# Kernel optimization log

Hardware: AMD Instinct MI355X
Metric: run time of the kernel (lower is better)

## Reference

```python
import jax, jax.numpy as jnp
import numpy as np

NUM_HEADS = 32
HEAD_DIM = 32  # hard-coded in the module


def _rope_sincos(seq_len, head_dim):
    # NOTE: module uses arange(0, head_dim)/head_dim (full dim, not the usual /2 stride)
    inv_freq = 1.0 / (10000.0 ** (jnp.arange(0, head_dim, dtype=jnp.float32) / head_dim))
    freqs = jnp.outer(jnp.arange(seq_len, dtype=jnp.float32), inv_freq)  # [S, D]
    # original repeats over heads then reshapes -> identical values per head,
    # so broadcasting with shape [1, S, 1, D] is equivalent.
    return jnp.sin(freqs)[None, :, None, :], jnp.cos(freqs)[None, :, None, :]


def _apply_rope(x, sin, cos):
    x1, x2 = jnp.split(x, 2, axis=-1)
    x_rot = jnp.concatenate([-x2, x1], axis=-1)
    return x * cos + x_rot * sin


def setup_inputs() -> dict:
    key = jax.random.key(0)
    B, S, H, D = 2, 2048, NUM_HEADS, HEAD_DIM
    dm = H * D
    k1, k2 = jax.random.split(key)
    x = jax.random.normal(k1, (B, S, dm), dtype=jnp.float32)
    W_qkv = jax.random.normal(k2, (dm, 3 * dm), dtype=jnp.float32) / np.sqrt(dm).astype(np.float32)
    mask = jnp.tril(jnp.ones((S, S), dtype=bool))[None, None]  # causal, [1,1,S,S]
    return {"x": x, "W_qkv": W_qkv, "mask": mask}


def reference(x, W_qkv, mask):
    B, S, dm = x.shape
    H, D = NUM_HEADS, HEAD_DIM
    qkv = x @ W_qkv  # [B, S, 3*H*D], no bias
    q, k, v = jnp.split(qkv, 3, axis=-1)
    q = q.reshape(B, S, H, D)
    k = k.reshape(B, S, H, D)
    v = v.reshape(B, S, H, D)

    sin, cos = _rope_sincos(S, D)
    q = _apply_rope(q, sin, cos)
    k = _apply_rope(k, sin, cos)

    # [B, H, S, D]
    q = q.transpose(0, 2, 1, 3)
    k = k.transpose(0, 2, 1, 3)
    v = v.transpose(0, 2, 1, 3)

    scale = 1.0 / np.sqrt(D).astype(np.float32)
    attn = jnp.einsum('bhqd,bhkd->bhqk', q, k) * scale  # [B, H, S, S]
    attn = jnp.where(mask, attn, jnp.float32(-jnp.inf))
    attn = jax.nn.softmax(attn, axis=-1)
    out = jnp.einsum('bhqk,bhkd->bhqd', attn, v)  # [B, H, S, D]
    return out.transpose(0, 2, 1, 3).reshape(B, S, H * D)
```

## Files before the change

kernel.cpp:

```cpp
#include <hip/hip_runtime.h>
#include <cstdint>
#include <cstddef>

#define BB 2
#define SS 2048
#define HH 32
#define DD 32
#define DM 1024
#define MROWS 4096
#define NQKV 3072

#define QSCALE 0.25503486f

typedef __attribute__((ext_vector_type(8))) short bf16x8;
typedef __attribute__((ext_vector_type(4))) float f32x4;
typedef __attribute__((address_space(1))) unsigned int gu32;
typedef __attribute__((address_space(3))) unsigned int lu32;

__device__ __forceinline__ unsigned short f2bf(float f) {
    union { float f; unsigned int u; } v;
    v.f = f;
    unsigned int u = v.u;
    u += 0x7fffu + ((u >> 16) & 1u);
    return (unsigned short)(u >> 16);
}

__device__ __forceinline__ unsigned int cvt_pk_bf16(float a, float b) {
    unsigned int r;
    asm("v_cvt_pk_bf16_f32 %0, %1, %2" : "=v"(r) : "v"(a), "v"(b));
    return r;
}
__device__ __forceinline__ unsigned short bf1(float a) {
    return (unsigned short)cvt_pk_bf16(a, a);
}

__global__ __launch_bounds__(256) void prep_k(
        const float* __restrict__ x, const float* __restrict__ w,
        unsigned short* __restrict__ xb, unsigned short* __restrict__ wT,
        float* __restrict__ tk, float* __restrict__ tq) {
    __shared__ unsigned short tile[64][65];
    const int blk = blockIdx.x;
    const int tid = threadIdx.x;
    if (blk < 4096) {
        const int i = blk * 256 + tid;
        float4 v = ((const float4*)x)[i];
        ushort4 o;
        o.x = f2bf(v.x); o.y = f2bf(v.y); o.z = f2bf(v.z); o.w = f2bf(v.w);
        ((ushort4*)xb)[i] = o;
    } else if (blk < 4864) {
        const int bx = blk - 4096;
        const int n0 = (bx % 48) * 64;
        const int k0 = (bx / 48) * 64;
        const int tx = tid & 63;
        const int ty = tid >> 6;
        for (int i = ty; i < 64; i += 4)
            tile[i][tx] = f2bf(w[(size_t)(k0 + i) * NQKV + n0 + tx]);
        __syncthreads();
        for (int i = ty; i < 64; i += 4)
            wT[(size_t)(n0 + i) * 1024 + k0 + tx] = tile[tx][i];
    } else {
        const int i = (blk - 4864) * 256 + tid;
        const int s = i >> 4, dl = i & 15;
        const float inv1 = exp2f((float)dl * -0.41524101186092029f);
        const float inv2 = exp2f((float)(dl + 16) * -0.41524101186092029f);
        float s1, c1, s2, c2;
        sincosf((float)s * inv1, &s1, &c1);
        sincosf((float)s * inv2, &s2, &c2);
        float4 vk = {s1, c1, s2, c2};
        float4 vq = {s1 * QSCALE, c1 * QSCALE, s2 * QSCALE, c2 * QSCALE};
        ((float4*)tk)[i] = vk;
        ((float4*)tq)[i] = vq;
    }
}

__global__ __launch_bounds__(256) void qkv_gemm_k(
        const unsigned short* __restrict__ xb,
        const unsigned short* __restrict__ wTp,
        const float4* __restrict__ tk, const float4* __restrict__ tq,
        unsigned short* __restrict__ qbuf,
        unsigned short* __restrict__ kbuf,
        unsigned short* __restrict__ vtbuf) {
    __shared__ unsigned short smem[2 * 8192];
    const int m0 = blockIdx.x * 128;
    const int n0 = blockIdx.y * 128;
    const int tid = threadIdx.x;
    const int w = tid >> 6, lane = tid & 63;
    const int quad = lane >> 4, l16 = lane & 15;
    const int wr = w >> 1, wc = w & 1;

    f32x4 acc[4][4];
#pragma unroll
    for (int i = 0; i < 4; ++i)
#pragma unroll
        for (int j = 0; j < 4; ++j)
            acc[i][j] = (f32x4){0.f, 0.f, 0.f, 0.f};

    const int G = (lane & 56) | ((lane ^ (lane >> 3)) & 7);
    const int goff = (G >> 2) * 1024 + (G & 3) * 8;
    const int Gr = l16 * 4 + quad;
    const int L = Gr ^ ((Gr >> 3) & 7);
    const int roff = L * 8;

#define QKV_STAGE(k0, buf)                                                          \
    do {                                                                            \
        unsigned short* As_ = smem + (buf) * 8192;                                  \
        unsigned short* Bs_ = As_ + 4096;                                           \
        _Pragma("unroll")                                                           \
        for (int q = 0; q < 2; ++q) {                                               \
            const int seg = w * 2 + q;                                              \
            const unsigned short* ga = xb  + (size_t)(m0 + seg * 16) * 1024 + (k0) + goff; \
            const unsigned short* gb = wTp + (size_t)(n0 + seg * 16) * 1024 + (k0) + goff; \
            __builtin_amdgcn_global_load_lds((gu32*)ga, (lu32*)(As_ + seg * 512), 16, 0, 0); \
            __builtin_amdgcn_global_load_lds((gu32*)gb, (lu32*)(Bs_ + seg * 512), 16, 0, 0); \
        }                                                                           \
    } while (0)

    QKV_STAGE(0, 0);
    __syncthreads();
    int cur = 0;
    for (int kt = 0; kt < 32; ++kt) {
        if (kt < 31) QKV_STAGE((kt + 1) * 32, cur ^ 1);
        const unsigned short* As = smem + cur * 8192;
        const unsigned short* Bs = As + 4096;
        bf16x8 af[4], bfv[4];
#pragma unroll
        for (int i = 0; i < 4; ++i)
            af[i] = *(const bf16x8*)(As + (wr * 4 + i) * 512 + roff);
#pragma unroll
        for (int j = 0; j < 4; ++j)
            bfv[j] = *(const bf16x8*)(Bs + (wc * 4 + j) * 512 + roff);
#pragma unroll
        for (int i = 0; i < 4; ++i)
#pragma unroll
            for (int j = 0; j < 4; ++j)
                acc[i][j] = __builtin_amdgcn_mfma_f32_16x16x32_bf16(af[i], bfv[j], acc[i][j], 0, 0, 0);
        __syncthreads();
        cur ^= 1;
    }
#undef QKV_STAGE

    const int sec = n0 >> 10;
    const int rowb = m0 + wr * 64;
    const int colb = n0 + wc * 64;
    if (sec < 2) {
        unsigned short* dst = (sec == 0) ? qbuf : kbuf;
        const float4* tab = (sec == 0) ? tq : tk;
        const int h0 = (colb & 1023) >> 5;
        const int h1 = ((colb + 32) & 1023) >> 5;
#pragma unroll
        for (int i = 0; i < 4; ++i) {
#pragma unroll
            for (int r = 0; r < 4; ++r) {
                const int row = rowb + i * 16 + quad * 4 + r;
                const int bb = row >> 11, s = row & 2047;
                const float4 t = tab[s * 16 + l16];
                unsigned short* pb = dst + ((size_t)(bb * 32) * 2048 + s) * 32;
                {
                    const float x1 = acc[i][0][r], x2 = acc[i][1][r];
                    unsigned short* p = pb + (size_t)h0 * (2048 * 32);
                    p[l16]      = bf1(x1 * t.y - x2 * t.x);
                    p[l16 + 16] = bf1(x2 * t.w + x1 * t.z);
                }
                {
                    const float x1 = acc[i][2][r], x2 = acc[i][3][r];
                    unsigned short* p = pb + (size_t)h1 * (2048 * 32);
                    p[l16]      = bf1(x1 * t.y - x2 * t.x);
                    p[l16 + 16] = bf1(x2 * t.w + x1 * t.z);
                }
            }
        }
    } else {
        __syncthreads();
        unsigned short* tw = smem + w * 2048;
        const int bbi = rowb >> 11;
        const int srow = rowb & 2047;
        const int colB = colb - 2048;
#pragma unroll
        for (int j = 0; j < 4; ++j) {
#pragma unroll
            for (int i = 0; i < 4; ++i) {
                uint2 pk;
                pk.x = cvt_pk_bf16(acc[i][j][0], acc[i][j][1]);
                pk.y = cvt_pk_bf16(acc[i][j][2], acc[i][j][3]);
                *(uint2*)&tw[l16 * 66 + i * 16 + quad * 4] = pk;
            }
#pragma unroll
            for (int c = 0; c < 16; ++c) {
                const int col = colB + j * 16 + c;
                const int hh = col >> 5, d = col & 31;
                vtbuf[((size_t)(bbi * 32 + hh) * 32 + d) * 2048 + srow + lane] = tw[c * 66 + lane];
            }
        }
    }
}

__global__ __launch_bounds__(256) void attn_k(
        const unsigned short* __restrict__ qb,
        const unsigned short* __restrict__ kb,
        const unsigned short* __restrict__ vt,
        float* __restrict__ out) {
    __shared__ unsigned short Pl[4][2][32][40];
    const int tid = threadIdx.x;
    const int w = tid >> 6, lane = tid & 63;
    const int quad = lane >> 4, l16 = lane & 15;
    const int i = blockIdx.x;
    const int xcd = i & 7;
    const int slot = i >> 3;
    const int bh = ((slot & 7) << 3) | xcd;
    const int pr = slot >> 3;
    const int b = bh >> 5, h = bh & 31;

    const unsigned short* qbase = qb + (size_t)bh * 2048 * 32;
    const unsigned short* kbase = kb + (size_t)bh * 2048 * 32;
    const unsigned short* vbase = vt + (size_t)bh * 32 * 2048;
    const f32x4 fz = {0.f, 0.f, 0.f, 0.f};

    for (int ph = 0; ph < 2; ++ph) {
        const int qw = (ph == 0) ? (pr * 128 + w * 32)
                                 : ((15 - pr) * 128 + (3 - w) * 32);
        const int nkt = (qw >> 5) + 1;

        bf16x8 qf0 = *(const bf16x8*)(qbase + (size_t)(qw + l16) * 32 + quad * 8);
        bf16x8 qf1 = *(const bf16x8*)(qbase + (size_t)(qw + 16 + l16) * 32 + quad * 8);

        f32x4 a00 = fz, a01 = fz, a10 = fz, a11 = fz;
        float ls0 = 0.f, ls1 = 0.f;

        const unsigned short* kp0 = kbase + (size_t)l16 * 32 + quad * 8;
        const unsigned short* kp1 = kbase + (size_t)(16 + l16) * 32 + quad * 8;
        const unsigned short* vp0 = vbase + (size_t)l16 * 2048 + quad * 8;
        const unsigned short* vp1 = vbase + (size_t)(16 + l16) * 2048 + quad * 8;

        bf16x8 kc0 = *(const bf16x8*)kp0;
        bf16x8 kc1 = *(const bf16x8*)kp1;
        bf16x8 vc0 = *(const bf16x8*)vp0;
        bf16x8 vc1 = *(const bf16x8*)vp1;

        f32x4 s00 = __builtin_amdgcn_mfma_f32_16x16x32_bf16(kc0, qf0, fz, 0, 0, 0);
        f32x4 s01 = __builtin_amdgcn_mfma_f32_16x16x32_bf16(kc0, qf1, fz, 0, 0, 0);
        f32x4 s10 = __builtin_amdgcn_mfma_f32_16x16x32_bf16(kc1, qf0, fz, 0, 0, 0);
        f32x4 s11 = __builtin_amdgcn_mfma_f32_16x16x32_bf16(kc1, qf1, fz, 0, 0, 0);

        for (int kt = 0; kt < nkt - 1; ++kt) {
            kp0 += 1024; kp1 += 1024; vp0 += 32; vp1 += 32;
            bf16x8 kn0 = *(const bf16x8*)kp0;
            bf16x8 kn1 = *(const bf16x8*)kp1;
            bf16x8 vn0 = *(const bf16x8*)vp0;
            bf16x8 vn1 = *(const bf16x8*)vp1;

            unsigned short (*plw)[40] = Pl[w][kt & 1];
            {
                float p0 = __builtin_amdgcn_exp2f(s00[0]), p1 = __builtin_amdgcn_exp2f(s00[1]);
                float p2 = __builtin_amdgcn_exp2f(s00[2]), p3 = __builtin_amdgcn_exp2f(s00[3]);
                ls0 += (p0 + p1) + (p2 + p3);
                uint2 pk; pk.x = cvt_pk_bf16(p0, p1); pk.y = cvt_pk_bf16(p2, p3);
                *(uint2*)&plw[l16][quad * 4] = pk;
            }
            {
                float p0 = __builtin_amdgcn_exp2f(s01[0]), p1 = __builtin_amdgcn_exp2f(s01[1]);
                float p2 = __builtin_amdgcn_exp2f(s01[2]), p3 = __builtin_amdgcn_exp2f(s01[3]);
                ls1 += (p0 + p1) + (p2 + p3);
                uint2 pk; pk.x = cvt_pk_bf16(p0, p1); pk.y = cvt_pk_bf16(p2, p3);
                *(uint2*)&plw[16 + l16][quad * 4] = pk;
            }
            {
                float p0 = __builtin_amdgcn_exp2f(s10[0]), p1 = __builtin_amdgcn_exp2f(s10[1]);
                float p2 = __builtin_amdgcn_exp2f(s10[2]), p3 = __builtin_amdgcn_exp2f(s10[3]);
                ls0 += (p0 + p1) + (p2 + p3);
                uint2 pk; pk.x = cvt_pk_bf16(p0, p1); pk.y = cvt_pk_bf16(p2, p3);
                *(uint2*)&plw[l16][16 + quad * 4] = pk;
            }
            {
                float p0 = __builtin_amdgcn_exp2f(s11[0]), p1 = __builtin_amdgcn_exp2f(s11[1]);
                float p2 = __builtin_amdgcn_exp2f(s11[2]), p3 = __builtin_amdgcn_exp2f(s11[3]);
                ls1 += (p0 + p1) + (p2 + p3);
                uint2 pk; pk.x = cvt_pk_bf16(p0, p1); pk.y = cvt_pk_bf16(p2, p3);
                *(uint2*)&plw[16 + l16][16 + quad * 4] = pk;
            }

            bf16x8 pf0 = *(const bf16x8*)&plw[l16][quad * 8];
            bf16x8 pf1 = *(const bf16x8*)&plw[16 + l16][quad * 8];
            a00 = __builtin_amdgcn_mfma_f32_16x16x32_bf16(vc0, pf0, a00, 0, 0, 0);
            a01 = __builtin_amdgcn_mfma_f32_16x16x32_bf16(vc0, pf1, a01, 0, 0, 0);
            a10 = __builtin_amdgcn_mfma_f32_16x16x32_bf16(vc1, pf0, a10, 0, 0, 0);
            a11 = __builtin_amdgcn_mfma_f32_16x16x32_bf16(vc1, pf1, a11, 0, 0, 0);

            s00 = __builtin_amdgcn_mfma_f32_16x16x32_bf16(kn0, qf0, fz, 0, 0, 0);
            s01 = __builtin_amdgcn_mfma_f32_16x16x32_bf16(kn0, qf1, fz, 0, 0, 0);
            s10 = __builtin_amdgcn_mfma_f32_16x16x32_bf16(kn1, qf0, fz, 0, 0, 0);
            s11 = __builtin_amdgcn_mfma_f32_16x16x32_bf16(kn1, qf1, fz, 0, 0, 0);

            vc0 = vn0; vc1 = vn1;
        }

        {
            unsigned short (*plw)[40] = Pl[w][(nkt - 1) & 1];
            {
                float p[4];
#pragma unroll
                for (int r = 0; r < 4; ++r)
                    p[r] = (quad * 4 + r > l16) ? 0.f : __builtin_amdgcn_exp2f(s00[r]);
                ls0 += (p[0] + p[1]) + (p[2] + p[3]);
                uint2 pk; pk.x = cvt_pk_bf16(p[0], p[1]); pk.y = cvt_pk_bf16(p[2], p[3]);
                *(uint2*)&plw[l16][quad * 4] = pk;
            }
            {
                float p0 = __builtin_amdgcn_exp2f(s01[0]), p1 = __builtin_amdgcn_exp2f(s01[1]);
                float p2 = __builtin_amdgcn_exp2f(s01[2]), p3 = __builtin_amdgcn_exp2f(s01[3]);
                ls1 += (p0 + p1) + (p2 + p3);
                uint2 pk; pk.x = cvt_pk_bf16(p0, p1); pk.y = cvt_pk_bf16(p2, p3);
                *(uint2*)&plw[16 + l16][quad * 4] = pk;
            }
            {
                uint2 pk; pk.x = 0; pk.y = 0;
                *(uint2*)&plw[l16][16 + quad * 4] = pk;
            }
            {
                float p[4];
#pragma unroll
                for (int r = 0; r < 4; ++r)
                    p[r] = (quad * 4 + r > l16) ? 0.f : __builtin_amdgcn_exp2f(s11[r]);
                ls1 += (p[0] + p[1]) + (p[2] + p[3]);
                uint2 pk; pk.x = cvt_pk_bf16(p[0], p[1]); pk.y = cvt_pk_bf16(p[2], p[3]);
                *(uint2*)&plw[16 + l16][16 + quad * 4] = pk;
            }

            bf16x8 pf0 = *(const bf16x8*)&plw[l16][quad * 8];
            bf16x8 pf1 = *(const bf16x8*)&plw[16 + l16][quad * 8];
            a00 = __builtin_amdgcn_mfma_f32_16x16x32_bf16(vc0, pf0, a00, 0, 0, 0);
            a01 = __builtin_amdgcn_mfma_f32_16x16x32_bf16(vc0, pf1, a01, 0, 0, 0);
            a10 = __builtin_amdgcn_mfma_f32_16x16x32_bf16(vc1, pf0, a10, 0, 0, 0);
            a11 = __builtin_amdgcn_mfma_f32_16x16x32_bf16(vc1, pf1, a11, 0, 0, 0);
        }

        float l0 = ls0; l0 += __shfl_xor(l0, 16); l0 += __shfl_xor(l0, 32);
        float l1 = ls1; l1 += __shfl_xor(l1, 16); l1 += __shfl_xor(l1, 32);
        const float inv0 = 1.f / l0, inv1 = 1.f / l1;

        float* ot = (float*)&Pl[w][0][0][0];
        {
            f32x4 t;
            t = a00; t[0]*=inv0; t[1]*=inv0; t[2]*=inv0; t[3]*=inv0;
            *(f32x4*)&ot[(l16) * 36 + quad * 4] = t;
            t = a10; t[0]*=inv0; t[1]*=inv0; t[2]*=inv0; t[3]*=inv0;
            *(f32x4*)&ot[(l16) * 36 + 16 + quad * 4] = t;
            t = a01; t[0]*=inv1; t[1]*=inv1; t[2]*=inv1; t[3]*=inv1;
            *(f32x4*)&ot[(16 + l16) * 36 + quad * 4] = t;
            t = a11; t[0]*=inv1; t[1]*=inv1; t[2]*=inv1; t[3]*=inv1;
            *(f32x4*)&ot[(16 + l16) * 36 + 16 + quad * 4] = t;
        }
        const int dd = lane & 31, qpar = lane >> 5;
        float* ob = out + (size_t)(b * 2048 + qw) * 1024 + h * 32;
#pragma unroll
        for (int i2 = 0; i2 < 16; ++i2) {
            const int qloc = i2 * 2 + qpar;
            ob[(size_t)qloc * 1024 + dd] = ot[qloc * 36 + dd];
        }
    }
}

extern "C" void kernel_launch(void* const* d_in, const int* in_sizes, int n_in,
                              void* d_out, int out_size, void* d_ws, size_t ws_size,
                              hipStream_t stream) {
    (void)in_sizes; (void)n_in; (void)out_size; (void)ws_size;
    const float* x = (const float*)d_in[0];
    const float* wq = (const float*)d_in[1];
    float* out = (float*)d_out;

    unsigned short* xb = (unsigned short*)d_ws;
    unsigned short* wT = xb + (size_t)MROWS * DM;
    unsigned short* qb = wT + (size_t)NQKV * DM;
    unsigned short* kb = qb + (size_t)BB * HH * SS * DD;
    unsigned short* vt = kb + (size_t)BB * HH * SS * DD;
    float* tk = (float*)(vt + (size_t)BB * HH * SS * DD);
    float* tq = tk + (size_t)SS * 16 * 4;

    prep_k<<<dim3(4992), dim3(256), 0, stream>>>(x, wq, xb, wT, tk, tq);
    qkv_gemm_k<<<dim3(MROWS / 128, NQKV / 128), dim3(256), 0, stream>>>(
        xb, wT, (const float4*)tk, (const float4*)tq, qb, kb, vt);
    attn_k<<<dim3(BB * HH * 8), dim3(256), 0, stream>>>(qb, kb, vt, out);
}
```

Before: 178.9 us.

## Split attention key loop into two interleaved accumulator streams per wave

The attention inner loop now splits key tiles into two independent streams (even and odd tiles), each with its own accumulators, row sums, prefetch pointers and LDS P buffers. The two streams are interleaved so the MFMA, exp and LDS work of one can overlap with the other, and the partial results are summed at the end. The diagonal masked tile is handled by whichever stream owns it. This doubles accumulator and prefetch register pressure and LDS footprint, which may reduce occupancy.

```diff
diff --git a/kernel.cpp b/kernel.cpp
--- a/kernel.cpp
+++ b/kernel.cpp
@@ -194,12 +194,104 @@
     }
 }
 
+#define ATTN_TILE(KC0, KC1, VC0, VC1, KP0, KP1, VP0, VP1, A00, A01, A10, A11, LS0, LS1, PLW) \
+    {                                                                                \
+        KP0 += 2048; KP1 += 2048; VP0 += 64; VP1 += 64;                              \
+        bf16x8 kn0 = *(const bf16x8*)KP0;                                            \
+        bf16x8 kn1 = *(const bf16x8*)KP1;                                            \
+        bf16x8 vn0 = *(const bf16x8*)VP0;                                            \
+        bf16x8 vn1 = *(const bf16x8*)VP1;                                            \
+        f32x4 s00 = __builtin_amdgcn_mfma_f32_16x16x32_bf16(KC0, qf0, fz, 0, 0, 0);  \
+        f32x4 s01 = __builtin_amdgcn_mfma_f32_16x16x32_bf16(KC0, qf1, fz, 0, 0, 0);  \
+        f32x4 s10 = __builtin_amdgcn_mfma_f32_16x16x32_bf16(KC1, qf0, fz, 0, 0, 0);  \
+        f32x4 s11 = __builtin_amdgcn_mfma_f32_16x16x32_bf16(KC1, qf1, fz, 0, 0, 0);  \
+        unsigned short (*plw)[40] = PLW;                                             \
+        {                                                                            \
+            float p0 = __builtin_amdgcn_exp2f(s00[0]), p1 = __builtin_amdgcn_exp2f(s00[1]); \
+            float p2 = __builtin_amdgcn_exp2f(s00[2]), p3 = __builtin_amdgcn_exp2f(s00[3]); \
+            LS0 += (p0 + p1) + (p2 + p3);                                            \
+            uint2 pk; pk.x = cvt_pk_bf16(p0, p1); pk.y = cvt_pk_bf16(p2, p3);        \
+            *(uint2*)&plw[l16][quad * 4] = pk;                                       \
+        }                                                                            \
+        {                                                                            \
+            float p0 = __builtin_amdgcn_exp2f(s01[0]), p1 = __builtin_amdgcn_exp2f(s01[1]); \
+            float p2 = __builtin_amdgcn_exp2f(s01[2]), p3 = __builtin_amdgcn_exp2f(s01[3]); \
+            LS1 += (p0 + p1) + (p2 + p3);                                            \
+            uint2 pk; pk.x = cvt_pk_bf16(p0, p1); pk.y = cvt_pk_bf16(p2, p3);        \
+            *(uint2*)&plw[16 + l16][quad * 4] = pk;                                  \
+        }                                                                            \
+        {                                                                            \
+            float p0 = __builtin_amdgcn_exp2f(s10[0]), p1 = __builtin_amdgcn_exp2f(s10[1]); \
+            float p2 = __builtin_amdgcn_exp2f(s10[2]), p3 = __builtin_amdgcn_exp2f(s10[3]); \
+            LS0 += (p0 + p1) + (p2 + p3);                                            \
+            uint2 pk; pk.x = cvt_pk_bf16(p0, p1); pk.y = cvt_pk_bf16(p2, p3);        \
+            *(uint2*)&plw[l16][16 + quad * 4] = pk;                                  \
+        }                                                                            \
+        {                                                                            \
+            float p0 = __builtin_amdgcn_exp2f(s11[0]), p1 = __builtin_amdgcn_exp2f(s11[1]); \
+            float p2 = __builtin_amdgcn_exp2f(s11[2]), p3 = __builtin_amdgcn_exp2f(s11[3]); \
+            LS1 += (p0 + p1) + (p2 + p3);                                            \
+            uint2 pk; pk.x = cvt_pk_bf16(p0, p1); pk.y = cvt_pk_bf16(p2, p3);        \
+            *(uint2*)&plw[16 + l16][16 + quad * 4] = pk;                             \
+        }                                                                            \
+        bf16x8 pf0 = *(const bf16x8*)&plw[l16][quad * 8];                            \
+        bf16x8 pf1 = *(const bf16x8*)&plw[16 + l16][quad * 8];                       \
+        A00 = __builtin_amdgcn_mfma_f32_16x16x32_bf16(VC0, pf0, A00, 0, 0, 0);       \
+        A01 = __builtin_amdgcn_mfma_f32_16x16x32_bf16(VC0, pf1, A01, 0, 0, 0);       \
+        A10 = __builtin_amdgcn_mfma_f32_16x16x32_bf16(VC1, pf0, A10, 0, 0, 0);       \
+        A11 = __builtin_amdgcn_mfma_f32_16x16x32_bf16(VC1, pf1, A11, 0, 0, 0);       \
+        KC0 = kn0; KC1 = kn1; VC0 = vn0; VC1 = vn1;                                  \
+    }
+
+#define ATTN_DIAG(KC0, KC1, VC0, VC1, A00, A01, A10, A11, LS0, LS1, PLW)             \
+    {                                                                                \
+        f32x4 s00 = __builtin_amdgcn_mfma_f32_16x16x32_bf16(KC0, qf0, fz, 0, 0, 0);  \
+        f32x4 s01 = __builtin_amdgcn_mfma_f32_16x16x32_bf16(KC0, qf1, fz, 0, 0, 0);  \
+        f32x4 s11 = __builtin_amdgcn_mfma_f32_16x16x32_bf16(KC1, qf1, fz, 0, 0, 0);  \
+        unsigned short (*plw)[40] = PLW;                                             \
+        {                                                                            \
+            float p[4];                                                              \
+            _Pragma("unroll")                                                        \
+            for (int r = 0; r < 4; ++r)                                              \
+                p[r] = (quad * 4 + r > l16) ? 0.f : __builtin_amdgcn_exp2f(s00[r]);  \
+            LS0 += (p[0] + p[1]) + (p[2] + p[3]);                                    \
+            uint2 pk; pk.x = cvt_pk_bf16(p[0], p[1]); pk.y = cvt_pk_bf16(p[2], p[3]); \
+            *(uint2*)&plw[l16][quad * 4] = pk;                                       \
+        }                                                                            \
+        {                                                                            \
+            float p0 = __builtin_amdgcn_exp2f(s01[0]), p1 = __builtin_amdgcn_exp2f(s01[1]); \
+            float p2 = __builtin_amdgcn_exp2f(s01[2]), p3 = __builtin_amdgcn_exp2f(s01[3]); \
+            LS1 += (p0 + p1) + (p2 + p3);                                            \
+            uint2 pk; pk.x = cvt_pk_bf16(p0, p1); pk.y = cvt_pk_bf16(p2, p3);        \
+            *(uint2*)&plw[16 + l16][quad * 4] = pk;                                  \
+        }                                                                            \
+        {                                                                            \
+            uint2 pk; pk.x = 0; pk.y = 0;                                            \
+            *(uint2*)&plw[l16][16 + quad * 4] = pk;                                  \
+        }                                                                            \
+        {                                                                            \
+            float p[4];                                                              \
+            _Pragma("unroll")                                                        \
+            for (int r = 0; r < 4; ++r)                                              \
+                p[r] = (quad * 4 + r > l16) ? 0.f : __builtin_amdgcn_exp2f(s11[r]);  \
+            LS1 += (p[0] + p[1]) + (p[2] + p[3]);                                    \
+            uint2 pk; pk.x = cvt_pk_bf16(p[0], p[1]); pk.y = cvt_pk_bf16(p[2], p[3]); \
+            *(uint2*)&plw[16 + l16][16 + quad * 4] = pk;                             \
+        }                                                                            \
+        bf16x8 pf0 = *(const bf16x8*)&plw[l16][quad * 8];                            \
+        bf16x8 pf1 = *(const bf16x8*)&plw[16 + l16][quad * 8];                       \
+        A00 = __builtin_amdgcn_mfma_f32_16x16x32_bf16(VC0, pf0, A00, 0, 0, 0);       \
+        A01 = __builtin_amdgcn_mfma_f32_16x16x32_bf16(VC0, pf1, A01, 0, 0, 0);       \
+        A10 = __builtin_amdgcn_mfma_f32_16x16x32_bf16(VC1, pf0, A10, 0, 0, 0);       \
+        A11 = __builtin_amdgcn_mfma_f32_16x16x32_bf16(VC1, pf1, A11, 0, 0, 0);       \
+    }
+
 __global__ __launch_bounds__(256) void attn_k(
         const unsigned short* __restrict__ qb,
         const unsigned short* __restrict__ kb,
         const unsigned short* __restrict__ vt,
         float* __restrict__ out) {
-    __shared__ unsigned short Pl[4][2][32][40];
+    __shared__ unsigned short Pl[4][2][2][32][40];
     const int tid = threadIdx.x;
     const int w = tid >> 6, lane = tid & 63;
     const int quad = lane >> 4, l16 = lane & 15;
@@ -219,125 +311,61 @@
         const int qw = (ph == 0) ? (pr * 128 + w * 32)
                                  : ((15 - pr) * 128 + (3 - w) * 32);
         const int nkt = (qw >> 5) + 1;
+        const int m = nkt - 1;
+        const int mA = (m + 1) >> 1;
+        const int mB = m >> 1;
 
         bf16x8 qf0 = *(const bf16x8*)(qbase + (size_t)(qw + l16) * 32 + quad * 8);
         bf16x8 qf1 = *(const bf16x8*)(qbase + (size_t)(qw + 16 + l16) * 32 + quad * 8);
 
-        f32x4 a00 = fz, a01 = fz, a10 = fz, a11 = fz;
-        float ls0 = 0.f, ls1 = 0.f;
-
-        const unsigned short* kp0 = kbase + (size_t)l16 * 32 + quad * 8;
-        const unsigned short* kp1 = kbase + (size_t)(16 + l16) * 32 + quad * 8;
-        const unsigned short* vp0 = vbase + (size_t)l16 * 2048 + quad * 8;
-        const unsigned short* vp1 = vbase + (size_t)(16 + l16) * 2048 + quad * 8;
-
-        bf16x8 kc0 = *(const bf16x8*)kp0;
-        bf16x8 kc1 = *(const bf16x8*)kp1;
-        bf16x8 vc0 = *(const bf16x8*)vp0;
-        bf16x8 vc1 = *(const bf16x8*)vp1;
-
-        f32x4 s00 = __builtin_amdgcn_mfma_f32_16x16x32_bf16(kc0, qf0, fz, 0, 0, 0);
-        f32x4 s01 = __builtin_amdgcn_mfma_f32_16x16x32_bf16(kc0, qf1, fz, 0, 0, 0);
-        f32x4 s10 = __builtin_amdgcn_mfma_f32_16x16x32_bf16(kc1, qf0, fz, 0, 0, 0);
-        f32x4 s11 = __builtin_amdgcn_mfma_f32_16x16x32_bf16(kc1, qf1, fz, 0, 0, 0);
-
-        for (int kt = 0; kt < nkt - 1; ++kt) {
-            kp0 += 1024; kp1 += 1024; vp0 += 32; vp1 += 32;
-            bf16x8 kn0 = *(const bf16x8*)kp0;
-            bf16x8 kn1 = *(const bf16x8*)kp1;
-            bf16x8 vn0 = *(const bf16x8*)vp0;
-            bf16x8 vn1 = *(const bf16x8*)vp1;
-
-            unsigned short (*plw)[40] = Pl[w][kt & 1];
-            {
-                float p0 = __builtin_amdgcn_exp2f(s00[0]), p1 = __builtin_amdgcn_exp2f(s00[1]);
-                float p2 = __builtin_amdgcn_exp2f(s00[2]), p3 = __builtin_amdgcn_exp2f(s00[3]);
-                ls0 += (p0 + p1) + (p2 + p3);
-                uint2 pk; pk.x = cvt_pk_bf16(p0, p1); pk.y = cvt_pk_bf16(p2, p3);
-                *(uint2*)&plw[l16][quad * 4] = pk;
+        f32x4 aA00 = fz, aA01 = fz, aA10 = fz, aA11 = fz;
+        float lsA0 = 0.f, lsA1 = 0.f;
+        const unsigned short* kpA0 = kbase + (size_t)l16 * 32 + quad * 8;
+        const unsigned short* kpA1 = kbase + (size_t)(16 + l16) * 32 + quad * 8;
+        const unsigned short* vpA0 = vbase + (size_t)l16 * 2048 + quad * 8;
+        const unsigned short* vpA1 = vbase + (size_t)(16 + l16) * 2048 + quad * 8;
+        bf16x8 kcA0 = *(const bf16x8*)kpA0;
+        bf16x8 kcA1 = *(const bf16x8*)kpA1;
+        bf16x8 vcA0 = *(const bf16x8*)vpA0;
+        bf16x8 vcA1 = *(const bf16x8*)vpA1;
+
+        f32x4 aB00 = fz, aB01 = fz, aB10 = fz, aB11 = fz;
+        float lsB0 = 0.f, lsB1 = 0.f;
+        const unsigned short* kpB0 = kpA0 + 1024;
+        const unsigned short* kpB1 = kpA1 + 1024;
+        const unsigned short* vpB0 = vpA0 + 32;
+        const unsigned short* vpB1 = vpA1 + 32;
+        bf16x8 kcB0 = *(const bf16x8*)kpB0;
+        bf16x8 kcB1 = *(const bf16x8*)kpB1;
+        bf16x8 vcB0 = *(const bf16x8*)vpB0;
+        bf16x8 vcB1 = *(const bf16x8*)vpB1;
+
+        for (int it = 0; it < mA; ++it) {
+            ATTN_TILE(kcA0, kcA1, vcA0, vcA1, kpA0, kpA1, vpA0, vpA1,
+                      aA00, aA01, aA10, aA11, lsA0, lsA1, Pl[w][0][it & 1]);
+            if (it < mB) {
+                ATTN_TILE(kcB0, kcB1, vcB0, vcB1, kpB0, kpB1, vpB0, vpB1,
+                          aB00, aB01, aB10, aB11, lsB0, lsB1, Pl[w][1][it & 1]);
             }
-            {
-                float p0 = __builtin_amdgcn_exp2f(s01[0]), p1 = __builtin_amdgcn_exp2f(s01[1]);
-                float p2 = __builtin_amdgcn_exp2f(s01[2]), p3 = __builtin_amdgcn_exp2f(s01[3]);
-                ls1 += (p0 + p1) + (p2 + p3);
-                uint2 pk; pk.x = cvt_pk_bf16(p0, p1); pk.y = cvt_pk_bf16(p2, p3);
-                *(uint2*)&plw[16 + l16][quad * 4] = pk;
-            }
-            {
-                float p0 = __builtin_amdgcn_exp2f(s10[0]), p1 = __builtin_amdgcn_exp2f(s10[1]);
-                float p2 = __builtin_amdgcn_exp2f(s10[2]), p3 = __builtin_amdgcn_exp2f(s10[3]);
-                ls0 += (p0 + p1) + (p2 + p3);
-                uint2 pk; pk.x = cvt_pk_bf16(p0, p1); pk.y = cvt_pk_bf16(p2, p3);
-                *(uint2*)&plw[l16][16 + quad * 4] = pk;
-            }
-            {
-                float p0 = __builtin_amdgcn_exp2f(s11[0]), p1 = __builtin_amdgcn_exp2f(s11[1]);
-                float p2 = __builtin_amdgcn_exp2f(s11[2]), p3 = __builtin_amdgcn_exp2f(s11[3]);
-                ls1 += (p0 + p1) + (p2 + p3);
-                uint2 pk; pk.x = cvt_pk_bf16(p0, p1); pk.y = cvt_pk_bf16(p2, p3);
-                *(uint2*)&plw[16 + l16][16 + quad * 4] = pk;
-            }
-
-            bf16x8 pf0 = *(const bf16x8*)&plw[l16][quad * 8];
-            bf16x8 pf1 = *(const bf16x8*)&plw[16 + l16][quad * 8];
-            a00 = __builtin_amdgcn_mfma_f32_16x16x32_bf16(vc0, pf0, a00, 0, 0, 0);
-            a01 = __builtin_amdgcn_mfma_f32_16x16x32_bf16(vc0, pf1, a01, 0, 0, 0);
-            a10 = __builtin_amdgcn_mfma_f32_16x16x32_bf16(vc1, pf0, a10, 0, 0, 0);
-            a11 = __builtin_amdgcn_mfma_f32_16x16x32_bf16(vc1, pf1, a11, 0, 0, 0);
-
-            s00 = __builtin_amdgcn_mfma_f32_16x16x32_bf16(kn0, qf0, fz, 0, 0, 0);
-            s01 = __builtin_amdgcn_mfma_f32_16x16x32_bf16(kn0, qf1, fz, 0, 0, 0);
-            s10 = __builtin_amdgcn_mfma_f32_16x16x32_bf16(kn1, qf0, fz, 0, 0, 0);
-            s11 = __builtin_amdgcn_mfma_f32_16x16x32_bf16(kn1, qf1, fz, 0, 0, 0);
-
-            vc0 = vn0; vc1 = vn1;
-        }
-
-        {
-            unsigned short (*plw)[40] = Pl[w][(nkt - 1) & 1];
-            {
-                float p[4];
-#pragma unroll
-                for (int r = 0; r < 4; ++r)
-                    p[r] = (quad * 4 + r > l16) ? 0.f : __builtin_amdgcn_exp2f(s00[r]);
-                ls0 += (p[0] + p[1]) + (p[2] + p[3]);
-                uint2 pk; pk.x = cvt_pk_bf16(p[0], p[1]); pk.y = cvt_pk_bf16(p[2], p[3]);
-                *(uint2*)&plw[l16][quad * 4] = pk;
-            }
-            {
-                float p0 = __builtin_amdgcn_exp2f(s01[0]), p1 = __builtin_amdgcn_exp2f(s01[1]);
-                float p2 = __builtin_amdgcn_exp2f(s01[2]), p3 = __builtin_amdgcn_exp2f(s01[3]);
-                ls1 += (p0 + p1) + (p2 + p3);
-                uint2 pk; pk.x = cvt_pk_bf16(p0, p1); pk.y = cvt_pk_bf16(p2, p3);
-                *(uint2*)&plw[16 + l16][quad * 4] = pk;
-            }
-            {
-                uint2 pk; pk.x = 0; pk.y = 0;
-                *(uint2*)&plw[l16][16 + quad * 4] = pk;
-            }
-            {
-                float p[4];
-#pragma unroll
-                for (int r = 0; r < 4; ++r)
-                    p[r] = (quad * 4 + r > l16) ? 0.f : __builtin_amdgcn_exp2f(s11[r]);
-                ls1 += (p[0] + p[1]) + (p[2] + p[3]);
-                uint2 pk; pk.x = cvt_pk_bf16(p[0], p[1]); pk.y = cvt_pk_bf16(p[2], p[3]);
-                *(uint2*)&plw[16 + l16][16 + quad * 4] = pk;
-            }
-
-            bf16x8 pf0 = *(const bf16x8*)&plw[l16][quad * 8];
-            bf16x8 pf1 = *(const bf16x8*)&plw[16 + l16][quad * 8];
-            a00 = __builtin_amdgcn_mfma_f32_16x16x32_bf16(vc0, pf0, a00, 0, 0, 0);
-            a01 = __builtin_amdgcn_mfma_f32_16x16x32_bf16(vc0, pf1, a01, 0, 0, 0);
-            a10 = __builtin_amdgcn_mfma_f32_16x16x32_bf16(vc1, pf0, a10, 0, 0, 0);
-            a11 = __builtin_amdgcn_mfma_f32_16x16x32_bf16(vc1, pf1, a11, 0, 0, 0);
-        }
+        }
+
+        if (m & 1) {
+            ATTN_DIAG(kcB0, kcB1, vcB0, vcB1, aB00, aB01, aB10, aB11,
+                      lsB0, lsB1, Pl[w][1][mB & 1]);
+        } else {
+            ATTN_DIAG(kcA0, kcA1, vcA0, vcA1, aA00, aA01, aA10, aA11,
+                      lsA0, lsA1, Pl[w][0][mA & 1]);
+        }
+
+        f32x4 a00 = aA00 + aB00, a01 = aA01 + aB01;
+        f32x4 a10 = aA10 + aB10, a11 = aA11 + aB11;
+        float ls0 = lsA0 + lsB0, ls1 = lsA1 + lsB1;
 
         float l0 = ls0; l0 += __shfl_xor(l0, 16); l0 += __shfl_xor(l0, 32);
         float l1 = ls1; l1 += __shfl_xor(l1, 16); l1 += __shfl_xor(l1, 32);
         const float inv0 = 1.f / l0, inv1 = 1.f / l1;
 
-        float* ot = (float*)&Pl[w][0][0][0];
+        float* ot = (float*)&Pl[w][0][0][0][0];
         {
             f32x4 t;
             t = a00; t[0]*=inv0; t[1]*=inv0; t[2]*=inv0; t[3]*=inv0;
```

Measured after the change: 179.1 us. About the same (+0.1%).
